# Performance work log

Hardware: AMD Instinct MI355X
Metric: run time of the kernel (lower is better)

The kernel has to match this reference:

```python
import jax, jax.numpy as jnp
import numpy as np
import math

B, T, C, H = 2, 2048, 1024, 16
D = C // H  # head dim = 64

def setup_inputs() -> dict:
    key = jax.random.key(0)
    ks = jax.random.split(key, 9)
    s = 0.02
    return {
        "x": jax.random.normal(ks[0], (B, T, C), dtype=jnp.float32),
        "Wq": jax.random.normal(ks[1], (C, C), dtype=jnp.float32) * s,
        "bq": jax.random.normal(ks[2], (C,), dtype=jnp.float32) * s,
        "Wk": jax.random.normal(ks[3], (C, C), dtype=jnp.float32) * s,
        "bk": jax.random.normal(ks[4], (C,), dtype=jnp.float32) * s,
        "Wv": jax.random.normal(ks[5], (C, C), dtype=jnp.float32) * s,
        "bv": jax.random.normal(ks[6], (C,), dtype=jnp.float32) * s,
        "Wo": jax.random.normal(ks[7], (C, C), dtype=jnp.float32) * s,
        "bo": jax.random.normal(ks[8], (C,), dtype=jnp.float32) * s,
    }

def reference(x, Wq, bq, Wk, bk, Wv, bv, Wo, bo):
    # x: [B, T, C]; torch Linear is y = x @ W.T + b
    Bv_, Tv_, Cv_ = x.shape
    q = (x @ Wq.T + bq).reshape(Bv_, Tv_, H, D)
    k = (x @ Wk.T + bk).reshape(Bv_, Tv_, H, D)
    v = (x @ Wv.T + bv).reshape(Bv_, Tv_, H, D)
    scale = 1.0 / math.sqrt(D)
    # [B, H, Tq, Tk] attention scores
    att = jnp.einsum("bqhd,bkhd->bhqk", q, k) * scale
    causal = jnp.tril(jnp.ones((Tv_, Tv_), dtype=bool))  # [T, T]
    att = jnp.where(causal[None, None, :, :], att, -jnp.inf)
    att = jax.nn.softmax(att, axis=-1)
    y = jnp.einsum("bhqk,bkhd->bqhd", att, v).reshape(Bv_, Tv_, Cv_)
    return y @ Wo.T + bo
```

## Files before the change

kernel.cpp:

```cpp
#include <hip/hip_runtime.h>
#include <hip/hip_bf16.h>
#include <cstdint>
#include <cstddef>

typedef __attribute__((ext_vector_type(8))) short short8;
typedef __attribute__((ext_vector_type(4))) float f32x4;
typedef unsigned int u32;

#define MFMA(a,b,c) __builtin_amdgcn_mfma_f32_16x16x32_bf16(a,b,c,0,0,0)

__device__ __forceinline__ void gload_lds16(const void* gptr, void* lptr) {
  __builtin_amdgcn_global_load_lds((const __attribute__((address_space(1))) u32*)gptr,
                                   (__attribute__((address_space(3))) u32*)lptr, 16, 0, 0);
}

template<int N> __device__ __forceinline__ void vm_wait() {
  asm volatile("s_waitcnt vmcnt(%0)" :: "n"(N) : "memory");
}

__device__ __forceinline__ void barrier_sync() {
  asm volatile("" ::: "memory");
  __builtin_amdgcn_s_barrier();
  asm volatile("" ::: "memory");
  __builtin_amdgcn_sched_barrier(0);
}

__device__ __forceinline__ unsigned short f2bf(float f) {
  __hip_bfloat16 h = __float2bfloat16(f);
  return *reinterpret_cast<unsigned short*>(&h);
}

__device__ __forceinline__ short8 ldg8(const unsigned short* p) {
  return *reinterpret_cast<const short8*>(p);
}

__device__ __forceinline__ u32 cvt_pk_bf16(float lo, float hi) {
  u32 r;
  asm("v_cvt_pk_bf16_f32 %0, %1, %2" : "=v"(r) : "v"(lo), "v"(hi));
  return r;
}

__global__ __launch_bounds__(256) void cvt_all_kernel(
    const float* __restrict__ x,
    const float* __restrict__ w0, const float* __restrict__ w1,
    const float* __restrict__ w2, const float* __restrict__ w3,
    unsigned short* __restrict__ xb,
    unsigned short* __restrict__ o0, unsigned short* __restrict__ o1,
    unsigned short* __restrict__ o2, unsigned short* __restrict__ o3)
{
  int id = blockIdx.x * blockDim.x + threadIdx.x;
  const float* in;
  unsigned short* out;
  int idx;
  if (id < 1048576) {
    in = x; out = xb; idx = id;
  } else {
    int r = id - 1048576;
    int z = r >> 18;
    idx = r & 262143;
    in  = (z == 0) ? w0 : (z == 1) ? w1 : (z == 2) ? w2 : w3;
    out = (z == 0) ? o0 : (z == 1) ? o1 : (z == 2) ? o2 : o3;
  }
  float4 f = reinterpret_cast<const float4*>(in)[idx];
  ushort4 o;
  o.x = f2bf(f.x); o.y = f2bf(f.y); o.z = f2bf(f.z); o.w = f2bf(f.w);
  reinterpret_cast<ushort4*>(out)[idx] = o;
}

template<int BM, int BN, int WM, int WN, bool F32OUT>
__device__ __forceinline__ void gemm2_body(
    const unsigned short* __restrict__ A,
    const unsigned short* __restrict__ W,
    const float* __restrict__ bias,
    unsigned short* __restrict__ outb, float* __restrict__ outf,
    int ldo, float oscale, int m0)
{
  constexpr int K = 1024, BK = 32, NT = K / BK;
  constexpr int NTHR = WM * WN * 64;
  constexpr int FM = BM / (WM * 16);
  constexpr int FN = BN / (WN * 16);
  constexpr int NLA = BM * BK * 2 / (NTHR * 16);
  constexpr int NLB = BN * BK * 2 / (NTHR * 16);
  constexpr int NLD = NLA + NLB;

  __shared__ unsigned short As[2][BM * BK];
  __shared__ unsigned short Ws[2][BN * BK];

  const int tid = threadIdx.x;
  const int lane = tid & 63;
  const int wave = tid >> 6;
  const int wm = wave / WN, wn = wave % WN;
  const int wr = wm * FM * 16, wc = wn * FN * 16;
  const int lr = lane >> 4, lc = lane & 15;

  f32x4 acc[FM][FN] = {};

  const char* Ab = (const char*)(A + (size_t)m0 * K);
  const char* Wb = (const char*)W;

#define STAGE(buf, k0)                                                            \
  {                                                                               \
    _Pragma("unroll")                                                             \
    for (int i = 0; i < NLA; ++i) {                                               \
      int L = (i * NTHR + tid) * 16;                                              \
      int row = L >> 6;                                                           \
      int col = L & 63;                                                           \
      gload_lds16(Ab + (size_t)row * 2048 + (k0) * 2 + col, (char*)&As[buf][0] + L); \
    }                                                                             \
    _Pragma("unroll")                                                             \
    for (int i = 0; i < NLB; ++i) {                                               \
      int L = (i * NTHR + tid) * 16;                                              \
      int row = L >> 6;                                                           \
      int col = L & 63;                                                           \
      gload_lds16(Wb + (size_t)row * 2048 + (k0) * 2 + col, (char*)&Ws[buf][0] + L); \
    }                                                                             \
  }

#define COMPUTE(buf)                                                              \
  {                                                                               \
    short8 af[FM], bf[FN];                                                        \
    _Pragma("unroll")                                                             \
    for (int m = 0; m < FM; ++m) {                                                \
      int row = wr + m * 16 + lc;                                                 \
      af[m] = *reinterpret_cast<const short8*>(                                   \
          (const char*)&As[buf][0] + row * 64 + lr * 16);                         \
    }                                                                             \
    _Pragma("unroll")                                                             \
    for (int n = 0; n < FN; ++n) {                                                \
      int row = wc + n * 16 + lc;                                                 \
      bf[n] = *reinterpret_cast<const short8*>(                                   \
          (const char*)&Ws[buf][0] + row * 64 + lr * 16);                         \
    }                                                                             \
    __builtin_amdgcn_s_setprio(1);                                                \
    _Pragma("unroll")                                                             \
    for (int m = 0; m < FM; ++m)                                                  \
      _Pragma("unroll")                                                           \
      for (int n = 0; n < FN; ++n)                                                \
        acc[m][n] = MFMA(af[m], bf[n], acc[m][n]);                                \
    __builtin_amdgcn_s_setprio(0);                                                \
  }

  STAGE(0, 0)
  STAGE(1, BK)
  int cur = 0;
#pragma unroll 1
  for (int kt = 0; kt < NT - 2; ++kt) {
    vm_wait<NLD>();
    barrier_sync();
    COMPUTE(cur)
    barrier_sync();
    STAGE(cur, (kt + 2) * BK)
    cur ^= 1;
  }
  vm_wait<NLD>();
  barrier_sync();
  COMPUTE(cur)
  cur ^= 1;
  vm_wait<0>();
  barrier_sync();
  COMPUTE(cur)

#undef STAGE
#undef COMPUTE

#pragma unroll
  for (int m = 0; m < FM; ++m)
#pragma unroll
    for (int n = 0; n < FN; ++n)
#pragma unroll
      for (int r = 0; r < 4; ++r) {
        int row = m0 + wr + m * 16 + lr * 4 + r;
        int col = wc + n * 16 + lc;
        float v = (acc[m][n][r] + bias[col]) * oscale;
        if (F32OUT) outf[(size_t)row * ldo + col] = v;
        else        outb[(size_t)row * ldo + col] = f2bf(v);
      }
}

__global__ __launch_bounds__(256, 3) void gemm_qkv5(
    const unsigned short* __restrict__ xb,
    const unsigned short* __restrict__ Wqb, const unsigned short* __restrict__ Wkb,
    const unsigned short* __restrict__ Wvb,
    const float* __restrict__ bq, const float* __restrict__ bk, const float* __restrict__ bv,
    unsigned short* __restrict__ Q, unsigned short* __restrict__ Ko, unsigned short* __restrict__ V)
{
  const int i = blockIdx.x;
  const int sw = (i & 7) * 96 + (i >> 3);
  const int z  = sw >> 8;
  const int rr = sw & 255;
  const int m0 = (rr >> 3) * 128;
  const int nr = (rr & 7) * 128;
  const unsigned short* W = ((z == 0) ? Wqb : (z == 1) ? Wkb : Wvb) + (size_t)nr * 1024;
  const float* bias = ((z == 0) ? bq : (z == 1) ? bk : bv) + nr;
  unsigned short* out = ((z == 0) ? Q : (z == 1) ? Ko : V) + nr;
  const float oscale = (z == 0) ? 0.18033688011112042f : 1.0f;
  gemm2_body<128, 128, 2, 2, false>(xb, W, bias, out, nullptr, 1024, oscale, m0);
}

__global__ __launch_bounds__(256, 2) void gemm_out3(
    const unsigned short* __restrict__ Y, const unsigned short* __restrict__ Wob,
    const float* __restrict__ bo, float* __restrict__ out)
{
  const int i = blockIdx.x;
  const int sw = (i & 7) * 64 + (i >> 3);
  const int by = sw >> 3;
  const int bx = sw & 7;
  const int m0 = by * 64;
  const int n0 = bx * 128;
  gemm2_body<64, 128, 2, 2, true>(Y, Wob + (size_t)n0 * 1024, bo + n0, nullptr, out + n0,
                                  1024, 1.0f, m0);
}

__global__ __launch_bounds__(256) void transpose_v(const unsigned short* __restrict__ V,
                                                   unsigned short* __restrict__ VT)
{
  __shared__ unsigned short tile[64 * 68];
  const int tb = blockIdx.x;
  const int bh = blockIdx.y;
  const int b = bh >> 4, h = bh & 15;
  const int tid = threadIdx.x;
  const int t0 = tb * 64;
#pragma unroll
  for (int i = 0; i < 4; ++i) {
    int e = (i * 256 + tid) * 4;
    int t = e >> 6, d = e & 63;
    ushort4 v = *reinterpret_cast<const ushort4*>(&V[((size_t)(b * 2048 + t0 + t)) * 1024 + h * 64 + d]);
    tile[t * 68 + d + 0] = v.x;
    tile[t * 68 + d + 1] = v.y;
    tile[t * 68 + d + 2] = v.z;
    tile[t * 68 + d + 3] = v.w;
  }
  __syncthreads();
#pragma unroll
  for (int i = 0; i < 4; ++i) {
    int e = (i * 256 + tid) * 4;
    int d = e >> 6, tc = e & 63;
    ushort4 w;
    w.x = tile[(tc + 0) * 68 + d];
    w.y = tile[(tc + 1) * 68 + d];
    w.z = tile[(tc + 2) * 68 + d];
    w.w = tile[(tc + 3) * 68 + d];
    *reinterpret_cast<ushort4*>(&VT[((size_t)(bh * 64 + d)) * 2048 + t0 + tc]) = w;
  }
}

__global__ __launch_bounds__(256, 2) void attn_kernel(
    const unsigned short* __restrict__ Q, const unsigned short* __restrict__ K,
    const unsigned short* __restrict__ VT, unsigned short* __restrict__ Y)
{
  __shared__ char smem[67584];

  const int i   = blockIdx.x;
  const int xcd = i & 7;
  const int bh  = xcd + 8 * ((i >> 3) & 3);
  const int qb  = 31 - (i >> 5);
  const int b = bh >> 4, h = bh & 15;
  const int tid = threadIdx.x;
  const int wave = tid >> 6;
  const int lane = tid & 63;
  const int lr = lane >> 4;
  const int lc = lane & 15;
  const float M = 4.0f;

  const unsigned short* Kbh = K + (size_t)b * 2048 * 1024 + h * 64;
  const unsigned short* Vbh = VT + (size_t)bh * 64 * 2048;
  char* PlB = smem + wave * 4096;

  const int q0 = qb * 64;

  short8 qf[4][2];
#pragma unroll
  for (int qg = 0; qg < 4; ++qg)
#pragma unroll
    for (int ds = 0; ds < 2; ++ds)
      qf[qg][ds] = ldg8(&Q[(size_t)(b * 2048 + q0 + qg * 16 + lc) * 1024 + h * 64 + ds * 32 + lr * 8]);

  f32x4 acc[4][4] = {};
  float lacc[4] = {};

  const int nt = 2 * qb + 2;

  short8 kfA[2][2], kfB[2][2];

#define LOADK(KF, t_)                                                             \
  {                                                                               \
    const int tkk = (t_) * 32;                                                    \
    _Pragma("unroll")                                                             \
    for (int kg = 0; kg < 2; ++kg)                                                \
      _Pragma("unroll")                                                           \
      for (int ds = 0; ds < 2; ++ds)                                              \
        KF[kg][ds] = ldg8(Kbh + (size_t)(tkk + kg * 16 + lc) * 1024 + ds * 32 + lr * 8); \
  }

#define COMPUTE(KF, t_)                                                           \
  {                                                                               \
    const int tk0 = (t_) * 32;                                                    \
    short8 vB[4];                                                                 \
    _Pragma("unroll")                                                             \
    for (int dg = 0; dg < 4; ++dg)                                                \
      vB[dg] = ldg8(Vbh + (size_t)(dg * 16 + lc) * 2048 + tk0 + lr * 8);          \
    f32x4 sa[2][4] = {};                                                          \
    __builtin_amdgcn_s_setprio(1);                                                \
    _Pragma("unroll")                                                             \
    for (int ds = 0; ds < 2; ++ds)                                                \
      _Pragma("unroll")                                                           \
      for (int kg = 0; kg < 2; ++kg)                                              \
        _Pragma("unroll")                                                         \
        for (int qg = 0; qg < 4; ++qg)                                            \
          sa[kg][qg] = MFMA(KF[kg][ds], qf[qg][ds], sa[kg][qg]);                  \
    __builtin_amdgcn_s_setprio(0);                                                \
    float p[2][4][4];                                                             \
    _Pragma("unroll")                                                             \
    for (int kg = 0; kg < 2; ++kg)                                                \
      _Pragma("unroll")                                                           \
      for (int qg = 0; qg < 4; ++qg)                                              \
        _Pragma("unroll")                                                         \
        for (int r = 0; r < 4; ++r)                                               \
          p[kg][qg][r] = __builtin_amdgcn_exp2f(sa[kg][qg][r] - M);               \
    if (tk0 + 31 > q0) {                                                          \
      _Pragma("unroll")                                                           \
      for (int kg = 0; kg < 2; ++kg)                                              \
        _Pragma("unroll")                                                         \
        for (int qg = 0; qg < 4; ++qg)                                            \
          _Pragma("unroll")                                                       \
          for (int r = 0; r < 4; ++r)                                             \
            if (tk0 + kg * 16 + lr * 4 + r > q0 + qg * 16 + lc) p[kg][qg][r] = 0.f; \
    }                                                                             \
    _Pragma("unroll")                                                             \
    for (int kg = 0; kg < 2; ++kg)                                                \
      _Pragma("unroll")                                                           \
      for (int qg = 0; qg < 4; ++qg)                                              \
        lacc[qg] += p[kg][qg][0] + p[kg][qg][1] + p[kg][qg][2] + p[kg][qg][3];    \
    _Pragma("unroll")                                                             \
    for (int kg = 0; kg < 2; ++kg)                                                \
      _Pragma("unroll")                                                           \
      for (int qg = 0; qg < 4; ++qg) {                                            \
        uint2 w;                                                                  \
        w.x = cvt_pk_bf16(p[kg][qg][0], p[kg][qg][1]);                            \
        w.y = cvt_pk_bf16(p[kg][qg][2], p[kg][qg][3]);                            \
        *reinterpret_cast<uint2*>(PlB + (qg * 16 + lc) * 64 +                     \
            ((kg * 32 + lr * 8) ^ ((lc & 3) << 4))) = w;                          \
      }                                                                           \
    short8 pA[4];                                                                 \
    _Pragma("unroll")                                                             \
    for (int qg = 0; qg < 4; ++qg)                                                \
      pA[qg] = *reinterpret_cast<const short8*>(PlB + (qg * 16 + lc) * 64 +       \
          ((lr * 16) ^ ((lc & 3) << 4)));                                         \
    __builtin_amdgcn_s_setprio(1);                                                \
    _Pragma("unroll")                                                             \
    for (int qg = 0; qg < 4; ++qg)                                                \
      _Pragma("unroll")                                                           \
      for (int dg = 0; dg < 4; ++dg)                                              \
        acc[qg][dg] = MFMA(pA[qg], vB[dg], acc[qg][dg]);                          \
    __builtin_amdgcn_s_setprio(0);                                                \
  }

  int t = wave;
  if (t < nt) LOADK(kfA, t)
#pragma unroll 1
  while (t < nt) {
    if (t + 4 < nt) LOADK(kfB, t + 4)
    COMPUTE(kfA, t)
    t += 4;
    if (t >= nt) break;
    if (t + 4 < nt) LOADK(kfA, t + 4)
    COMPUTE(kfB, t)
    t += 4;
  }

#undef LOADK
#undef COMPUTE

#pragma unroll
  for (int qg = 0; qg < 4; ++qg) {
    lacc[qg] += __shfl_xor(lacc[qg], 16);
    lacc[qg] += __shfl_xor(lacc[qg], 32);
  }

  __syncthreads();
  float* Ored = (float*)smem;
#pragma unroll
  for (int qg = 0; qg < 4; ++qg) {
#pragma unroll
    for (int dg = 0; dg < 4; ++dg)
#pragma unroll
      for (int r = 0; r < 4; ++r)
        Ored[(size_t)(wave * 64 + qg * 16 + lr * 4 + r) * 66 + dg * 16 + lc] = acc[qg][dg][r];
    if (lr == 0)
      Ored[(size_t)(wave * 64 + qg * 16 + lc) * 66 + 64] = lacc[qg];
  }
  __syncthreads();

  {
    const int qoff = lane & 15;
    const int dblk = lane >> 4;
    const int qrow = wave * 16 + qoff;
    float s[16];
#pragma unroll
    for (int j = 0; j < 16; ++j) s[j] = 0.f;
    float lsum = 0.f;
#pragma unroll
    for (int pz = 0; pz < 4; ++pz) {
      const float* rp = &Ored[(size_t)(pz * 64 + qrow) * 66];
#pragma unroll
      for (int j = 0; j < 16; ++j) s[j] += rp[dblk * 16 + j];
      lsum += rp[64];
    }
    float rl = __builtin_amdgcn_rcpf(lsum);
    unsigned short* yp = &Y[(size_t)(b * 2048 + q0 + qrow) * 1024 + h * 64 + dblk * 16];
#pragma unroll
    for (int j = 0; j < 16; j += 4) {
      ushort4 w;
      w.x = f2bf(s[j + 0] * rl);
      w.y = f2bf(s[j + 1] * rl);
      w.z = f2bf(s[j + 2] * rl);
      w.w = f2bf(s[j + 3] * rl);
      *reinterpret_cast<ushort4*>(yp + j) = w;
    }
  }
}

extern "C" void kernel_launch(void* const* d_in, const int* in_sizes, int n_in,
                              void* d_out, int out_size, void* d_ws, size_t ws_size,
                              hipStream_t stream)
{
  const float* x  = (const float*)d_in[0];
  const float* Wq = (const float*)d_in[1];
  const float* bq = (const float*)d_in[2];
  const float* Wk = (const float*)d_in[3];
  const float* bk = (const float*)d_in[4];
  const float* Wv = (const float*)d_in[5];
  const float* bv = (const float*)d_in[6];
  const float* Wo = (const float*)d_in[7];
  const float* bo = (const float*)d_in[8];
  float* out = (float*)d_out;

  char* ws = (char*)d_ws;
  unsigned short* xb  = (unsigned short*)(ws);
  unsigned short* Wqb = (unsigned short*)(ws + 8388608);
  unsigned short* Wkb = (unsigned short*)(ws + 8388608 + 2097152);
  unsigned short* Wvb = (unsigned short*)(ws + 8388608 + 2 * 2097152);
  unsigned short* Wob = (unsigned short*)(ws + 8388608 + 3 * 2097152);
  unsigned short* Qb  = (unsigned short*)(ws + 16777216);
  unsigned short* Kb  = (unsigned short*)(ws + 16777216 + 8388608);
  unsigned short* Vb  = (unsigned short*)(ws + 16777216 + 2 * 8388608);
  unsigned short* VTb = (unsigned short*)(ws + 16777216 + 3 * 8388608);
  unsigned short* Yb  = (unsigned short*)(ws + 16777216 + 4 * 8388608);

  cvt_all_kernel<<<8192, 256, 0, stream>>>(x, Wq, Wk, Wv, Wo, xb, Wqb, Wkb, Wvb, Wob);

  gemm_qkv5<<<768, 256, 0, stream>>>(xb, Wqb, Wkb, Wvb, bq, bk, bv, Qb, Kb, Vb);
  transpose_v<<<dim3(32, 32), 256, 0, stream>>>(Vb, VTb);
  attn_kernel<<<1024, 256, 0, stream>>>(Qb, Kb, VTb, Yb);
  gemm_out3<<<512, 256, 0, stream>>>(Yb, Wob, bo, out);
}
```

Baseline: 110.5 us.

## Halve attention LDS footprint to raise occupancy and drop softmax offset

After: 289.5 us. 2.62x slower.

```diff
diff --git a/kernel.cpp b/kernel.cpp
--- a/kernel.cpp
+++ b/kernel.cpp
@@ -244,11 +244,11 @@
   }
 }
 
-__global__ __launch_bounds__(256, 2) void attn_kernel(
+__global__ __launch_bounds__(256, 4) void attn_kernel(
     const unsigned short* __restrict__ Q, const unsigned short* __restrict__ K,
     const unsigned short* __restrict__ VT, unsigned short* __restrict__ Y)
 {
-  __shared__ char smem[67584];
+  __shared__ char smem[33792];
 
   const int i   = blockIdx.x;
   const int xcd = i & 7;
@@ -260,11 +260,10 @@
   const int lane = tid & 63;
   const int lr = lane >> 4;
   const int lc = lane & 15;
-  const float M = 4.0f;
 
   const unsigned short* Kbh = K + (size_t)b * 2048 * 1024 + h * 64;
   const unsigned short* Vbh = VT + (size_t)bh * 64 * 2048;
-  char* PlB = smem + wave * 4096;
+  char* PlB = smem + wave * 4608;
 
   const int q0 = qb * 64;
 
@@ -316,7 +315,7 @@
       for (int qg = 0; qg < 4; ++qg)                                              \
         _Pragma("unroll")                                                         \
         for (int r = 0; r < 4; ++r)                                               \
-          p[kg][qg][r] = __builtin_amdgcn_exp2f(sa[kg][qg][r] - M);               \
+          p[kg][qg][r] = __builtin_amdgcn_exp2f(sa[kg][qg][r]);                   \
     if (tk0 + 31 > q0) {                                                          \
       _Pragma("unroll")                                                           \
       for (int kg = 0; kg < 2; ++kg)                                              \
@@ -338,14 +337,12 @@
         uint2 w;                                                                  \
         w.x = cvt_pk_bf16(p[kg][qg][0], p[kg][qg][1]);                            \
         w.y = cvt_pk_bf16(p[kg][qg][2], p[kg][qg][3]);                            \
-        *reinterpret_cast<uint2*>(PlB + (qg * 16 + lc) * 64 +                     \
-            ((kg * 32 + lr * 8) ^ ((lc & 3) << 4))) = w;                          \
+        *reinterpret_cast<uint2*>(PlB + (qg * 16 + lc) * 72 + kg * 32 + lr * 8) = w; \
       }                                                                           \
     short8 pA[4];                                                                 \
     _Pragma("unroll")                                                             \
     for (int qg = 0; qg < 4; ++qg)                                                \
-      pA[qg] = *reinterpret_cast<const short8*>(PlB + (qg * 16 + lc) * 64 +       \
-          ((lr * 16) ^ ((lc & 3) << 4)));                                         \
+      pA[qg] = *reinterpret_cast<const short8*>(PlB + (qg * 16 + lc) * 72 + lr * 16); \
     __builtin_amdgcn_s_setprio(1);                                                \
     _Pragma("unroll")                                                             \
     for (int qg = 0; qg < 4; ++qg)                                                \
@@ -379,15 +376,30 @@
 
   __syncthreads();
   float* Ored = (float*)smem;
-#pragma unroll
-  for (int qg = 0; qg < 4; ++qg) {
-#pragma unroll
-    for (int dg = 0; dg < 4; ++dg)
-#pragma unroll
-      for (int r = 0; r < 4; ++r)
-        Ored[(size_t)(wave * 64 + qg * 16 + lr * 4 + r) * 66 + dg * 16 + lc] = acc[qg][dg][r];
-    if (lr == 0)
-      Ored[(size_t)(wave * 64 + qg * 16 + lc) * 66 + 64] = lacc[qg];
+  if (wave >= 2) {
+    float* dst = Ored + (size_t)(wave - 2) * 64 * 66;
+#pragma unroll
+    for (int qg = 0; qg < 4; ++qg) {
+#pragma unroll
+      for (int dg = 0; dg < 4; ++dg)
+#pragma unroll
+        for (int r = 0; r < 4; ++r)
+          dst[(size_t)(qg * 16 + lr * 4 + r) * 66 + dg * 16 + lc] = acc[qg][dg][r];
+      if (lr == 0) dst[(size_t)(qg * 16 + lc) * 66 + 64] = lacc[qg];
+    }
+  }
+  __syncthreads();
+  if (wave < 2) {
+    float* dst = Ored + (size_t)wave * 64 * 66;
+#pragma unroll
+    for (int qg = 0; qg < 4; ++qg) {
+#pragma unroll
+      for (int dg = 0; dg < 4; ++dg)
+#pragma unroll
+        for (int r = 0; r < 4; ++r)
+          dst[(size_t)(qg * 16 + lr * 4 + r) * 66 + dg * 16 + lc] += acc[qg][dg][r];
+      if (lr == 0) dst[(size_t)(qg * 16 + lc) * 66 + 64] += lacc[qg];
+    }
   }
   __syncthreads();
 
@@ -400,7 +412,7 @@
     for (int j = 0; j < 16; ++j) s[j] = 0.f;
     float lsum = 0.f;
 #pragma unroll
-    for (int pz = 0; pz < 4; ++pz) {
+    for (int pz = 0; pz < 2; ++pz) {
       const float* rp = &Ored[(size_t)(pz * 64 + qrow) * 66];
 #pragma unroll
       for (int j = 0; j < 16; ++j) s[j] += rp[dblk * 16 + j];
```
